# Performance work log

Measured on AMD Instinct MI355X. Metric: run time of the kernel, lower is better.

The kernel has to match this reference:

```python
import jax, jax.numpy as jnp
import numpy as np

B, S, D, H = 4, 2048, 1024, 16
DK = D // H

def setup_inputs() -> dict:
    key = jax.random.key(0)
    ks = jax.random.split(key, 11)
    s = 1.0 / np.sqrt(D)
    return {
        "query": jax.random.normal(ks[0], (B, S, D), jnp.float32),
        "key_": jax.random.normal(ks[1], (B, S, D), jnp.float32),
        "value": jax.random.normal(ks[2], (B, S, D), jnp.float32),
        "Wq": jax.random.uniform(ks[3], (D, D), jnp.float32, -s, s),
        "bq": jax.random.uniform(ks[4], (D,), jnp.float32, -s, s),
        "Wk": jax.random.uniform(ks[5], (D, D), jnp.float32, -s, s),
        "bk": jax.random.uniform(ks[6], (D,), jnp.float32, -s, s),
        "Wv": jax.random.uniform(ks[7], (D, D), jnp.float32, -s, s),
        "bv": jax.random.uniform(ks[8], (D,), jnp.float32, -s, s),
        "Wo": jax.random.uniform(ks[9], (D, D), jnp.float32, -s, s),
        "bo": jax.random.uniform(ks[10], (D,), jnp.float32, -s, s),
    }

def _split_heads(x):
    # [B,S,D] -> [B,H,S,DK]
    b, s, _ = x.shape
    return x.reshape(b, s, H, DK).transpose(0, 2, 1, 3)

def reference(query, key_, value, Wq, bq, Wk, bk, Wv, bv, Wo, bo):
    Q = _split_heads(query @ Wq.T + bq)
    K = _split_heads(key_ @ Wk.T + bk)
    V = _split_heads(value @ Wv.T + bv)
    scores = jnp.einsum('bhqd,bhkd->bhqk', Q, K) / np.sqrt(DK).astype(np.float32)
    attn = jax.nn.softmax(scores, axis=-1)
    ctx = jnp.einsum('bhqk,bhkd->bhqd', attn, V)  # [B,H,S,DK]
    ctx = ctx.transpose(0, 2, 1, 3).reshape(query.shape[0], -1, D)
    return ctx @ Wo.T + bo
```

## Files before the change

kernel.cpp:

```cpp
#include <hip/hip_runtime.h>
#include <hip/hip_bf16.h>
#include <math.h>


#define B_SZ   4
#define S_LEN  2048
#define D_DIM  1024
#define NH     16
#define DKD    64
#define M_TOT  (B_SZ * S_LEN)

typedef __bf16 bf16_t;
typedef bf16_t bf16x8 __attribute__((ext_vector_type(8)));
typedef bf16_t bf16x4 __attribute__((ext_vector_type(4)));
typedef float  f32x4  __attribute__((ext_vector_type(4)));

typedef __attribute__((address_space(1))) void gvoid;
typedef __attribute__((address_space(3))) void lvoid;

extern "C" __device__ float __ocml_native_exp2_f32(float);

__global__ __launch_bounds__(256)
void cvt_kernel(const float* __restrict__ src, bf16_t* __restrict__ dst, int n4)
{
    const int i = blockIdx.x * blockDim.x + threadIdx.x;
    if (i < n4) {
        f32x4 v = *(const f32x4*)(src + (size_t)i * 4);
        bf16x4 o;
        #pragma unroll
        for (int j = 0; j < 4; ++j) o[j] = (bf16_t)v[j];
        *(bf16x4*)(dst + (size_t)i * 4) = o;
    }
}

__global__ __launch_bounds__(256, 2)
void qkv_gemm(const float* __restrict__ Aq, const float* __restrict__ Ak,
              const float* __restrict__ Av,
              const bf16_t* __restrict__ Wqb, const bf16_t* __restrict__ Wkb,
              const bf16_t* __restrict__ Wvb,
              const float* __restrict__ bq, const float* __restrict__ bk,
              const float* __restrict__ bv,
              bf16_t* __restrict__ Qw, bf16_t* __restrict__ Kw,
              bf16_t* __restrict__ Vt, float qscale)
{
    constexpr int K = 1024, N = 1024;
    constexpr int BM = 128, BN = 128, BK = 32;

    __shared__ __align__(16) bf16_t lA[BM * BK];
    __shared__ __align__(16) bf16_t lB[BN * BK];

    const int z = blockIdx.z;
    const float* A  = (z == 0) ? Aq : (z == 1) ? Ak : Av;
    const bf16_t* W = (z == 0) ? Wqb : (z == 1) ? Wkb : Wvb;
    const float* bias = (z == 0) ? bq : (z == 1) ? bk : bv;
    const float scale = (z == 0) ? qscale : 1.0f;

    const int tid  = threadIdx.x;
    const int wave = tid >> 6;
    const int lane = tid & 63;

    const int row0 = blockIdx.x * BM;
    const int col0 = blockIdx.y * BN;

    const int wr = (wave >> 1) * 64;
    const int wc = (wave & 1) * 64;

    f32x4 acc[4][4] = {};

    const int frow = lane & 15;
    const int kq   = (lane >> 4) * 8;

    const int r0c = tid >> 2;
    const int k0c = (tid & 3) * 8;
    const int r1c = (256 + tid) >> 2;
    const int k1c = k0c;

    f32x4 pa[2][2];
    {
        const float* g0 = A + (size_t)(row0 + r0c) * K + k0c;
        const float* g1 = A + (size_t)(row0 + r1c) * K + k1c;
        pa[0][0] = *(const f32x4*)g0;  pa[0][1] = *(const f32x4*)(g0 + 4);
        pa[1][0] = *(const f32x4*)g1;  pa[1][1] = *(const f32x4*)(g1 + 4);
    }

    for (int k0 = 0; k0 < K; k0 += BK) {
        __syncthreads();
        #pragma unroll
        for (int p = 0; p < 2; ++p) {
            bf16x8 a8;
            #pragma unroll
            for (int j = 0; j < 4; ++j) {
                a8[j]     = (bf16_t)pa[p][0][j];
                a8[4 + j] = (bf16_t)pa[p][1][j];
            }
            *(bf16x8*)(lA + (p * 256 + tid) * 8) = a8;
        }
        #pragma unroll
        for (int c = 0; c < 2; ++c) {
            const int chunk = c * 4 + wave;
            const int e     = chunk * 512 + lane * 8;
            const int rr    = e >> 5;
            const int kk    = e & 31;
            __builtin_amdgcn_global_load_lds((gvoid*)(W + (size_t)(col0 + rr) * K + k0 + kk),
                                             (lvoid*)(lB + chunk * 512), 16, 0, 0);
        }
        __syncthreads();

        if (k0 + BK < K) {
            const float* g0 = A + (size_t)(row0 + r0c) * K + (k0 + BK) + k0c;
            const float* g1 = A + (size_t)(row0 + r1c) * K + (k0 + BK) + k1c;
            pa[0][0] = *(const f32x4*)g0;  pa[0][1] = *(const f32x4*)(g0 + 4);
            pa[1][0] = *(const f32x4*)g1;  pa[1][1] = *(const f32x4*)(g1 + 4);
        }

        bf16x8 af[4], bfr[4];
        #pragma unroll
        for (int i = 0; i < 4; ++i) {
            af[i]  = *(const bf16x8*)(lA + (wr + i * 16 + frow) * BK + kq);
            bfr[i] = *(const bf16x8*)(lB + (wc + i * 16 + frow) * BK + kq);
        }
        #pragma unroll
        for (int i = 0; i < 4; ++i)
            #pragma unroll
            for (int j = 0; j < 4; ++j)
                acc[i][j] = __builtin_amdgcn_mfma_f32_16x16x32_bf16(af[i], bfr[j], acc[i][j], 0, 0, 0);
    }

    const int rb   = (lane >> 4) * 4;
    const int ccol = lane & 15;
    #pragma unroll
    for (int j = 0; j < 4; ++j) {
        const int n = col0 + wc + j * 16 + ccol;
        const float bvv = bias[n];
        #pragma unroll
        for (int i = 0; i < 4; ++i) {
            const int m = row0 + wr + i * 16 + rb;
            if (z == 2) {
                bf16x4 o4;
                #pragma unroll
                for (int r = 0; r < 4; ++r) o4[r] = (bf16_t)(acc[i][j][r] + bvv);
                *(bf16x4*)(Vt + (size_t)n * M_TOT + m) = o4;
            } else {
                bf16_t* Cp = (z == 0) ? Qw : Kw;
                #pragma unroll
                for (int r = 0; r < 4; ++r)
                    Cp[(size_t)(m + r) * N + n] = (bf16_t)((acc[i][j][r] + bvv) * scale);
            }
        }
    }
}

__global__ __launch_bounds__(256, 2)
void gemm_out(const bf16_t* __restrict__ A, const bf16_t* __restrict__ Bt,
              const float* __restrict__ bias, float* __restrict__ C)
{
    constexpr int K = 1024, N = 1024;
    constexpr int BM = 128, BK = 32;

    __shared__ __align__(16) bf16_t lA[BM * BK];
    __shared__ __align__(16) bf16_t lB[128 * BK];

    const int tid  = threadIdx.x;
    const int wave = tid >> 6;
    const int lane = tid & 63;

    const int row0 = blockIdx.x * BM;
    const int col0 = blockIdx.y * 128;

    const int wr = (wave >> 1) * 64;
    const int wc = (wave & 1) * 64;

    f32x4 acc[4][4] = {};

    const int frow = lane & 15;
    const int kq   = (lane >> 4) * 8;

    for (int k0 = 0; k0 < K; k0 += BK) {
        __syncthreads();
        #pragma unroll
        for (int c = 0; c < 2; ++c) {
            const int chunk = c * 4 + wave;
            const int e     = chunk * 512 + lane * 8;
            const int r     = e >> 5;
            const int kk    = e & 31;
            __builtin_amdgcn_global_load_lds((gvoid*)(A + (size_t)(row0 + r) * K + k0 + kk),
                                             (lvoid*)(lA + chunk * 512), 16, 0, 0);
            __builtin_amdgcn_global_load_lds((gvoid*)(Bt + (size_t)(col0 + r) * K + k0 + kk),
                                             (lvoid*)(lB + chunk * 512), 16, 0, 0);
        }
        __syncthreads();

        bf16x8 af[4], bfr[4];
        #pragma unroll
        for (int i = 0; i < 4; ++i) {
            af[i]  = *(const bf16x8*)(lA + (wr + i * 16 + frow) * BK + kq);
            bfr[i] = *(const bf16x8*)(lB + (wc + i * 16 + frow) * BK + kq);
        }
        #pragma unroll
        for (int i = 0; i < 4; ++i)
            #pragma unroll
            for (int j = 0; j < 4; ++j)
                acc[i][j] = __builtin_amdgcn_mfma_f32_16x16x32_bf16(af[i], bfr[j], acc[i][j], 0, 0, 0);
    }

    const int rb   = (lane >> 4) * 4;
    const int ccol = lane & 15;
    #pragma unroll
    for (int j = 0; j < 4; ++j) {
        const int n = col0 + wc + j * 16 + ccol;
        const float bvv = bias[n];
        #pragma unroll
        for (int i = 0; i < 4; ++i) {
            const int m = row0 + wr + i * 16 + rb;
            #pragma unroll
            for (int r = 0; r < 4; ++r)
                C[(size_t)(m + r) * N + n] = acc[i][j][r] + bvv;
        }
    }
}

__global__ __launch_bounds__(256, 4)
void attn_mfma(const bf16_t* __restrict__ Qg, const bf16_t* __restrict__ Kg,
               const bf16_t* __restrict__ Vt, bf16_t* __restrict__ ctx)
{
    constexpr int PSTR = 72;
    __shared__ __align__(16) bf16_t lK[64 * PSTR];
    __shared__ __align__(16) bf16_t lV[64 * PSTR];
    __shared__ __align__(16) bf16_t lP[4][32 * PSTR];

    const int tid  = threadIdx.x;
    const int wave = tid >> 6;
    const int lane = tid & 63;
    const int qd   = lane >> 4;
    const int c    = lane & 15;

    const int bh   = blockIdx.x >> 4;
    const int qblk = blockIdx.x & 15;
    const int b    = bh >> 4;
    const int h    = bh & 15;

    const int q0 = qblk * 128 + wave * 32;

    const bf16_t* Qb = Qg + ((size_t)(b * S_LEN + q0)) * D_DIM + h * DKD;
    const bf16_t* Kb = Kg + ((size_t)(b * S_LEN)) * D_DIM + h * DKD;
    const bf16_t* Vb = Vt + ((size_t)(h * DKD)) * M_TOT + b * S_LEN;

    bf16_t* Pw = &lP[wave][0];

    bf16x8 qf[2][2];
    #pragma unroll
    for (int qt = 0; qt < 2; ++qt)
        #pragma unroll
        for (int ks = 0; ks < 2; ++ks)
            qf[qt][ks] = *(const bf16x8*)(Qb + (size_t)(qt * 16 + c) * D_DIM + ks * 32 + qd * 8);

    bf16x8 ones;
    #pragma unroll
    for (int i = 0; i < 8; ++i) ones[i] = (bf16_t)1.0f;

    f32x4 oacc[4][2] = {};
    f32x4 lacc[2]    = {};

    for (int kt = 0; kt < S_LEN; kt += 64) {
        __syncthreads();
        #pragma unroll
        for (int cc = 0; cc < 2; ++cc) {
            const int ch  = cc * 256 + tid;
            const int row = ch >> 3;
            const int c8  = ch & 7;
            bf16x8 kv = *(const bf16x8*)(Kb + (size_t)(kt + row) * D_DIM + c8 * 8);
            bf16x8 vv = *(const bf16x8*)(Vb + (size_t)row * M_TOT + kt + c8 * 8);
            *(bf16x8*)(lK + row * PSTR + c8 * 8) = kv;
            *(bf16x8*)(lV + row * PSTR + c8 * 8) = vv;
        }
        __syncthreads();

        bf16x8 kf[4][2];
        #pragma unroll
        for (int i = 0; i < 4; ++i)
            #pragma unroll
            for (int ks = 0; ks < 2; ++ks)
                kf[i][ks] = *(const bf16x8*)(lK + (i * 16 + c) * PSTR + ks * 32 + qd * 8);

        f32x4 st[4][2] = {};
        #pragma unroll
        for (int ks = 0; ks < 2; ++ks)
            #pragma unroll
            for (int i = 0; i < 4; ++i)
                #pragma unroll
                for (int qt = 0; qt < 2; ++qt)
                    st[i][qt] = __builtin_amdgcn_mfma_f32_16x16x32_bf16(kf[i][ks], qf[qt][ks], st[i][qt], 0, 0, 0);

        bf16x8 vf[4][2];
        #pragma unroll
        for (int fm = 0; fm < 4; ++fm)
            #pragma unroll
            for (int ks = 0; ks < 2; ++ks)
                vf[fm][ks] = *(const bf16x8*)(lV + (fm * 16 + c) * PSTR + ks * 32 + qd * 8);

        #pragma unroll
        for (int i = 0; i < 4; ++i)
            #pragma unroll
            for (int qt = 0; qt < 2; ++qt) {
                bf16x4 pw;
                #pragma unroll
                for (int r = 0; r < 4; ++r)
                    pw[r] = (bf16_t)__ocml_native_exp2_f32(st[i][qt][r]);
                *(bf16x4*)(Pw + (qt * 16 + c) * PSTR + i * 16 + qd * 4) = pw;
            }

        #pragma unroll
        for (int qn = 0; qn < 2; ++qn)
            #pragma unroll
            for (int ks = 0; ks < 2; ++ks) {
                bf16x8 pf = *(const bf16x8*)(Pw + (qn * 16 + c) * PSTR + ks * 32 + qd * 8);
                lacc[qn] = __builtin_amdgcn_mfma_f32_16x16x32_bf16(ones, pf, lacc[qn], 0, 0, 0);
                #pragma unroll
                for (int fm = 0; fm < 4; ++fm)
                    oacc[fm][qn] = __builtin_amdgcn_mfma_f32_16x16x32_bf16(vf[fm][ks], pf, oacc[fm][qn], 0, 0, 0);
            }
    }

    #pragma unroll
    for (int qn = 0; qn < 2; ++qn) {
        const float linv = 1.0f / lacc[qn][0];
        bf16_t* op = ctx + ((size_t)(b * S_LEN + q0 + qn * 16 + c)) * D_DIM + h * DKD + qd * 4;
        #pragma unroll
        for (int fm = 0; fm < 4; ++fm) {
            bf16x4 o4;
            #pragma unroll
            for (int r = 0; r < 4; ++r) o4[r] = (bf16_t)(oacc[fm][qn][r] * linv);
            *(bf16x4*)(op + fm * 16) = o4;
        }
    }
}

extern "C" void kernel_launch(void* const* d_in, const int* in_sizes, int n_in,
                              void* d_out, int out_size, void* d_ws, size_t ws_size,
                              hipStream_t stream)
{
    const float* query = (const float*)d_in[0];
    const float* key_  = (const float*)d_in[1];
    const float* value = (const float*)d_in[2];
    const float* Wq    = (const float*)d_in[3];
    const float* bq    = (const float*)d_in[4];
    const float* Wk    = (const float*)d_in[5];
    const float* bk    = (const float*)d_in[6];
    const float* Wv    = (const float*)d_in[7];
    const float* bv    = (const float*)d_in[8];
    const float* Wo    = (const float*)d_in[9];
    const float* bo    = (const float*)d_in[10];
    float* out = (float*)d_out;

    const size_t mat  = (size_t)M_TOT * D_DIM;
    const size_t wmat = (size_t)D_DIM * D_DIM;

    bf16_t* t0 = (bf16_t*)d_ws;
    bf16_t* w0 = t0 + mat;
    bf16_t* Qw = w0 + wmat;
    bf16_t* Kw = Qw + mat;
    bf16_t* Vt = Kw + mat;
    bf16_t* w1 = t0;
    bf16_t* w2 = t0 + wmat;

    const int gcvt_w = (int)(wmat / 4 / 256);
    const float qscale = 0.18033688011112042f;

    cvt_kernel<<<gcvt_w, 256, 0, stream>>>(Wq, w0, (int)(wmat / 4));
    cvt_kernel<<<gcvt_w, 256, 0, stream>>>(Wk, w1, (int)(wmat / 4));
    cvt_kernel<<<gcvt_w, 256, 0, stream>>>(Wv, w2, (int)(wmat / 4));

    qkv_gemm<<<dim3(M_TOT / 128, D_DIM / 128, 3), 256, 0, stream>>>(
        query, key_, value, w0, w1, w2, bq, bk, bv, Qw, Kw, Vt, qscale);

    attn_mfma<<<dim3(B_SZ * NH * (S_LEN / 128)), 256, 0, stream>>>(Qw, Kw, Vt, t0);

    cvt_kernel<<<gcvt_w, 256, 0, stream>>>(Wo, w0, (int)(wmat / 4));
    gemm_out<<<dim3(M_TOT / 128, D_DIM / 128), 256, 0, stream>>>(t0, w0, bo, out);
}
```

Baseline: 356.1 us.

## Double GEMM K-step, fuse weight conversions, swizzle attention block order

Both GEMM kernels now process a K-step of 64 per iteration, split into two 32-wide LDS sub-tiles. This halves the barrier and loop overhead per MFMA and puts more loads in flight. The three Q/K/V weight conversions merge into one launch with a z-grid, and the Wo conversion moves before the attention kernel. The attention kernel remaps block indices so that groups of heads are interleaved with query blocks, aiming for better K/V cache locality. The costs are higher register pressure from the larger prefetch and more LDS per block, which may reduce occupancy.

```diff
diff --git a/kernel.cpp b/kernel.cpp
--- a/kernel.cpp
+++ b/kernel.cpp
@@ -19,6 +19,23 @@
 typedef __attribute__((address_space(3))) void lvoid;
 
 extern "C" __device__ float __ocml_native_exp2_f32(float);
+
+__global__ __launch_bounds__(256)
+void cvt3_kernel(const float* __restrict__ s0, const float* __restrict__ s1,
+                 const float* __restrict__ s2, bf16_t* __restrict__ d0,
+                 bf16_t* __restrict__ d1, bf16_t* __restrict__ d2, int n4)
+{
+    const float* src = (blockIdx.z == 0) ? s0 : (blockIdx.z == 1) ? s1 : s2;
+    bf16_t*      dst = (blockIdx.z == 0) ? d0 : (blockIdx.z == 1) ? d1 : d2;
+    const int i = blockIdx.x * blockDim.x + threadIdx.x;
+    if (i < n4) {
+        f32x4 v = *(const f32x4*)(src + (size_t)i * 4);
+        bf16x4 o;
+        #pragma unroll
+        for (int j = 0; j < 4; ++j) o[j] = (bf16_t)v[j];
+        *(bf16x4*)(dst + (size_t)i * 4) = o;
+    }
+}
 
 __global__ __launch_bounds__(256)
 void cvt_kernel(const float* __restrict__ src, bf16_t* __restrict__ dst, int n4)
@@ -44,10 +61,10 @@
               bf16_t* __restrict__ Vt, float qscale)
 {
     constexpr int K = 1024, N = 1024;
-    constexpr int BM = 128, BN = 128, BK = 32;
-
-    __shared__ __align__(16) bf16_t lA[BM * BK];
-    __shared__ __align__(16) bf16_t lB[BN * BK];
+    constexpr int BM = 128, BK = 64;
+
+    __shared__ __align__(16) bf16_t lA[2][BM * 32];
+    __shared__ __align__(16) bf16_t lB[2][128 * 32];
 
     const int z = blockIdx.z;
     const float* A  = (z == 0) ? Aq : (z == 1) ? Ak : Av;
@@ -60,7 +77,7 @@
     const int lane = tid & 63;
 
     const int row0 = blockIdx.x * BM;
-    const int col0 = blockIdx.y * BN;
+    const int col0 = blockIdx.y * 128;
 
     const int wr = (wave >> 1) * 64;
     const int wc = (wave & 1) * 64;
@@ -70,60 +87,68 @@
     const int frow = lane & 15;
     const int kq   = (lane >> 4) * 8;
 
-    const int r0c = tid >> 2;
-    const int k0c = (tid & 3) * 8;
-    const int r1c = (256 + tid) >> 2;
-    const int k1c = k0c;
-
-    f32x4 pa[2][2];
-    {
-        const float* g0 = A + (size_t)(row0 + r0c) * K + k0c;
-        const float* g1 = A + (size_t)(row0 + r1c) * K + k1c;
-        pa[0][0] = *(const f32x4*)g0;  pa[0][1] = *(const f32x4*)(g0 + 4);
-        pa[1][0] = *(const f32x4*)g1;  pa[1][1] = *(const f32x4*)(g1 + 4);
+    const int arow = tid >> 3;
+    const int ak8  = (tid & 7) * 8;
+    const int asub = (tid >> 2) & 1;
+    const int akk  = (tid & 3) * 8;
+
+    f32x4 pa[4][2];
+    #pragma unroll
+    for (int p = 0; p < 4; ++p) {
+        const float* g = A + (size_t)(row0 + p * 32 + arow) * K + ak8;
+        pa[p][0] = *(const f32x4*)g;
+        pa[p][1] = *(const f32x4*)(g + 4);
     }
 
     for (int k0 = 0; k0 < K; k0 += BK) {
         __syncthreads();
         #pragma unroll
-        for (int p = 0; p < 2; ++p) {
+        for (int p = 0; p < 4; ++p) {
             bf16x8 a8;
             #pragma unroll
             for (int j = 0; j < 4; ++j) {
                 a8[j]     = (bf16_t)pa[p][0][j];
                 a8[4 + j] = (bf16_t)pa[p][1][j];
             }
-            *(bf16x8*)(lA + (p * 256 + tid) * 8) = a8;
-        }
-        #pragma unroll
-        for (int c = 0; c < 2; ++c) {
-            const int chunk = c * 4 + wave;
-            const int e     = chunk * 512 + lane * 8;
-            const int rr    = e >> 5;
-            const int kk    = e & 31;
-            __builtin_amdgcn_global_load_lds((gvoid*)(W + (size_t)(col0 + rr) * K + k0 + kk),
-                                             (lvoid*)(lB + chunk * 512), 16, 0, 0);
-        }
+            *(bf16x8*)(&lA[asub][(p * 32 + arow) * 32 + akk]) = a8;
+        }
+        #pragma unroll
+        for (int s = 0; s < 2; ++s)
+            #pragma unroll
+            for (int c = 0; c < 2; ++c) {
+                const int chunk = c * 4 + wave;
+                const int e     = chunk * 512 + lane * 8;
+                const int rr    = e >> 5;
+                const int kk    = e & 31;
+                __builtin_amdgcn_global_load_lds(
+                    (gvoid*)(W + (size_t)(col0 + rr) * K + k0 + 32 * s + kk),
+                    (lvoid*)(&lB[s][chunk * 512]), 16, 0, 0);
+            }
         __syncthreads();
 
         if (k0 + BK < K) {
-            const float* g0 = A + (size_t)(row0 + r0c) * K + (k0 + BK) + k0c;
-            const float* g1 = A + (size_t)(row0 + r1c) * K + (k0 + BK) + k1c;
-            pa[0][0] = *(const f32x4*)g0;  pa[0][1] = *(const f32x4*)(g0 + 4);
-            pa[1][0] = *(const f32x4*)g1;  pa[1][1] = *(const f32x4*)(g1 + 4);
-        }
-
-        bf16x8 af[4], bfr[4];
-        #pragma unroll
-        for (int i = 0; i < 4; ++i) {
-            af[i]  = *(const bf16x8*)(lA + (wr + i * 16 + frow) * BK + kq);
-            bfr[i] = *(const bf16x8*)(lB + (wc + i * 16 + frow) * BK + kq);
-        }
-        #pragma unroll
-        for (int i = 0; i < 4; ++i)
-            #pragma unroll
-            for (int j = 0; j < 4; ++j)
-                acc[i][j] = __builtin_amdgcn_mfma_f32_16x16x32_bf16(af[i], bfr[j], acc[i][j], 0, 0, 0);
+            #pragma unroll
+            for (int p = 0; p < 4; ++p) {
+                const float* g = A + (size_t)(row0 + p * 32 + arow) * K + (k0 + BK) + ak8;
+                pa[p][0] = *(const f32x4*)g;
+                pa[p][1] = *(const f32x4*)(g + 4);
+            }
+        }
+
+        #pragma unroll
+        for (int s = 0; s < 2; ++s) {
+            bf16x8 af[4], bfr[4];
+            #pragma unroll
+            for (int i = 0; i < 4; ++i) {
+                af[i]  = *(const bf16x8*)(&lA[s][(wr + i * 16 + frow) * 32 + kq]);
+                bfr[i] = *(const bf16x8*)(&lB[s][(wc + i * 16 + frow) * 32 + kq]);
+            }
+            #pragma unroll
+            for (int i = 0; i < 4; ++i)
+                #pragma unroll
+                for (int j = 0; j < 4; ++j)
+                    acc[i][j] = __builtin_amdgcn_mfma_f32_16x16x32_bf16(af[i], bfr[j], acc[i][j], 0, 0, 0);
+        }
     }
 
     const int rb   = (lane >> 4) * 4;
@@ -155,10 +180,10 @@
               const float* __restrict__ bias, float* __restrict__ C)
 {
     constexpr int K = 1024, N = 1024;
-    constexpr int BM = 128, BK = 32;
-
-    __shared__ __align__(16) bf16_t lA[BM * BK];
-    __shared__ __align__(16) bf16_t lB[128 * BK];
+    constexpr int BM = 128, BK = 64;
+
+    __shared__ __align__(16) bf16_t lA[2][BM * 32];
+    __shared__ __align__(16) bf16_t lB[2][128 * 32];
 
     const int tid  = threadIdx.x;
     const int wave = tid >> 6;
@@ -178,29 +203,36 @@
     for (int k0 = 0; k0 < K; k0 += BK) {
         __syncthreads();
         #pragma unroll
-        for (int c = 0; c < 2; ++c) {
-            const int chunk = c * 4 + wave;
-            const int e     = chunk * 512 + lane * 8;
-            const int r     = e >> 5;
-            const int kk    = e & 31;
-            __builtin_amdgcn_global_load_lds((gvoid*)(A + (size_t)(row0 + r) * K + k0 + kk),
-                                             (lvoid*)(lA + chunk * 512), 16, 0, 0);
-            __builtin_amdgcn_global_load_lds((gvoid*)(Bt + (size_t)(col0 + r) * K + k0 + kk),
-                                             (lvoid*)(lB + chunk * 512), 16, 0, 0);
-        }
-        __syncthreads();
-
-        bf16x8 af[4], bfr[4];
-        #pragma unroll
-        for (int i = 0; i < 4; ++i) {
-            af[i]  = *(const bf16x8*)(lA + (wr + i * 16 + frow) * BK + kq);
-            bfr[i] = *(const bf16x8*)(lB + (wc + i * 16 + frow) * BK + kq);
-        }
-        #pragma unroll
-        for (int i = 0; i < 4; ++i)
-            #pragma unroll
-            for (int j = 0; j < 4; ++j)
-                acc[i][j] = __builtin_amdgcn_mfma_f32_16x16x32_bf16(af[i], bfr[j], acc[i][j], 0, 0, 0);
+        for (int s = 0; s < 2; ++s)
+            #pragma unroll
+            for (int c = 0; c < 2; ++c) {
+                const int chunk = c * 4 + wave;
+                const int e     = chunk * 512 + lane * 8;
+                const int r     = e >> 5;
+                const int kk    = e & 31;
+                __builtin_amdgcn_global_load_lds(
+                    (gvoid*)(A + (size_t)(row0 + r) * K + k0 + 32 * s + kk),
+                    (lvoid*)(&lA[s][chunk * 512]), 16, 0, 0);
+                __builtin_amdgcn_global_load_lds(
+                    (gvoid*)(Bt + (size_t)(col0 + r) * K + k0 + 32 * s + kk),
+                    (lvoid*)(&lB[s][chunk * 512]), 16, 0, 0);
+            }
+        __syncthreads();
+
+        #pragma unroll
+        for (int s = 0; s < 2; ++s) {
+            bf16x8 af[4], bfr[4];
+            #pragma unroll
+            for (int i = 0; i < 4; ++i) {
+                af[i]  = *(const bf16x8*)(&lA[s][(wr + i * 16 + frow) * 32 + kq]);
+                bfr[i] = *(const bf16x8*)(&lB[s][(wc + i * 16 + frow) * 32 + kq]);
+            }
+            #pragma unroll
+            for (int i = 0; i < 4; ++i)
+                #pragma unroll
+                for (int j = 0; j < 4; ++j)
+                    acc[i][j] = __builtin_amdgcn_mfma_f32_16x16x32_bf16(af[i], bfr[j], acc[i][j], 0, 0, 0);
+        }
     }
 
     const int rb   = (lane >> 4) * 4;
@@ -234,8 +266,9 @@
     const int qd   = lane >> 4;
     const int c    = lane & 15;
 
-    const int bh   = blockIdx.x >> 4;
-    const int qblk = blockIdx.x & 15;
+    const int g    = blockIdx.x;
+    const int bh   = ((g >> 7) << 3) | (g & 7);
+    const int qblk = (g >> 3) & 15;
     const int b    = bh >> 4;
     const int h    = bh & 15;
 
@@ -366,15 +399,15 @@
     const int gcvt_w = (int)(wmat / 4 / 256);
     const float qscale = 0.18033688011112042f;
 
-    cvt_kernel<<<gcvt_w, 256, 0, stream>>>(Wq, w0, (int)(wmat / 4));
-    cvt_kernel<<<gcvt_w, 256, 0, stream>>>(Wk, w1, (int)(wmat / 4));
-    cvt_kernel<<<gcvt_w, 256, 0, stream>>>(Wv, w2, (int)(wmat / 4));
+    cvt3_kernel<<<dim3(gcvt_w, 1, 3), 256, 0, stream>>>(Wq, Wk, Wv, w0, w1, w2,
+                                                        (int)(wmat / 4));
 
     qkv_gemm<<<dim3(M_TOT / 128, D_DIM / 128, 3), 256, 0, stream>>>(
         query, key_, value, w0, w1, w2, bq, bk, bv, Qw, Kw, Vt, qscale);
 
+    cvt_kernel<<<gcvt_w, 256, 0, stream>>>(Wo, w0, (int)(wmat / 4));
+
     attn_mfma<<<dim3(B_SZ * NH * (S_LEN / 128)), 256, 0, stream>>>(Qw, Kw, Vt, t0);
 
-    cvt_kernel<<<gcvt_w, 256, 0, stream>>>(Wo, w0, (int)(wmat / 4));
     gemm_out<<<dim3(M_TOT / 128, D_DIM / 128), 256, 0, stream>>>(t0, w0, bo, out);
 }
```

After: 342.5 us. -3.8%, faster.
